# Optimization experiments

Measured on AMD Instinct MI355X. Metric: run time of the kernel, lower is better.

## Reference

```python
import jax, jax.numpy as jnp
import numpy as np

B, FEW, NN = 4096, 5, 64
D = 128            # embed_dim
NSYM = 100000
DM = 2 * D         # d_model = 256
DI = 2 * DM        # support-encoder inner = 512
H = 2 * DM         # LSTMCell hidden = 512
STEPS = 4          # process_steps


def setup_inputs() -> dict:
    key = jax.random.key(0)
    cnt = [0]
    def nk():
        cnt[0] += 1
        return jax.random.fold_in(key, cnt[0])
    def nrm(shape, scale=0.05):
        return jax.random.normal(nk(), shape, dtype=jnp.float32) * scale
    def ridx(shape):
        return jax.random.randint(nk(), shape, 0, NSYM, dtype=jnp.int32)
    inp = {}
    inp['q_l1'] = ridx((B, NN, 2)); inp['q_l2'] = ridx((B, NN, 2))
    inp['q_r1'] = ridx((B, NN, 2)); inp['q_r2'] = ridx((B, NN, 2))
    inp['s_l1'] = ridx((FEW, NN, 2)); inp['s_l2'] = ridx((FEW, NN, 2))
    inp['s_r1'] = ridx((FEW, NN, 2)); inp['s_r2'] = ridx((FEW, NN, 2))
    inp['q_deg_l'] = jax.random.randint(nk(), (B,), 1, NN, dtype=jnp.int32)
    inp['q_deg_r'] = jax.random.randint(nk(), (B,), 1, NN, dtype=jnp.int32)
    inp['s_deg_l'] = jax.random.randint(nk(), (FEW,), 1, NN, dtype=jnp.int32)
    inp['s_deg_r'] = jax.random.randint(nk(), (FEW,), 1, NN, dtype=jnp.int32)
    inp['emb'] = nrm((NSYM + 1, D)).at[NSYM].set(0.0)  # padding_idx row = 0
    inp['gcn_w'] = nrm((D, 2 * D))
    inp['gcn_wb'] = nrm((D,))
    inp['gcn_b'] = jnp.zeros((D,), jnp.float32)
    inp['hop_gate'] = jnp.ones((2,), jnp.float32)
    inp['attn_w'] = nrm((1, D))
    inp['attn_b'] = jnp.zeros((1,), jnp.float32)
    inp['p1_w'] = nrm((DI, DM)); inp['p1_b'] = jnp.zeros((DI,), jnp.float32)
    inp['p2_w'] = nrm((DM, DI)); inp['p2_b'] = jnp.zeros((DM,), jnp.float32)
    inp['ln_g'] = jnp.ones((DM,), jnp.float32); inp['ln_b'] = jnp.zeros((DM,), jnp.float32)
    inp['w_ih'] = nrm((4 * H, DM)); inp['w_hh'] = nrm((4 * H, H))
    inp['b_ih'] = jnp.zeros((4 * H,), jnp.float32); inp['b_hh'] = jnp.zeros((4 * H,), jnp.float32)
    return inp


def _neighbor_encoder(conn, emb, gcn_w, gcn_wb, gcn_b, attn_w, attn_b):
    # conn: [N, NN, 2] (relation id, entity id)
    e = emb[conn]                                     # [N, NN, 2, D]
    concat = e.reshape(conn.shape[0], conn.shape[1], 2 * D)  # cat(rel, ent)
    proj = concat @ gcn_w.T + gcn_wb + gcn_b          # [N, NN, D]
    scores = (proj @ attn_w.T + attn_b)[..., 0]       # [N, NN]
    w = jax.nn.softmax(scores, axis=1)[..., None]
    return jnp.tanh(jnp.sum(proj * w, axis=1))        # [N, D]


def _support_encoder(x, p1_w, p1_b, p2_w, p2_b, ln_g, ln_b):
    out = jax.nn.relu(x @ p1_w.T + p1_b) @ p2_w.T + p2_b
    z = out + x
    mu = jnp.mean(z, axis=-1, keepdims=True)
    var = jnp.var(z, axis=-1, keepdims=True)
    return (z - mu) / jnp.sqrt(var + 1e-6) * ln_g + ln_b


def _query_encoder(support_g, q, w_ih, w_hh, b_ih, b_hh):
    # matching-networks 'process' LSTM attention, STEPS fixed iterations
    h_r = jnp.zeros((q.shape[0], H), q.dtype)
    c = jnp.zeros_like(h_r)
    h = q
    for _ in range(STEPS):
        gates = q @ w_ih.T + b_ih + h_r @ w_hh.T + b_hh
        i, f, g, o = jnp.split(gates, 4, axis=-1)
        c = jax.nn.sigmoid(f) * c + jax.nn.sigmoid(i) * jnp.tanh(g)
        h_cell = jax.nn.sigmoid(o) * jnp.tanh(c)
        h = q + h_cell[:, :DM]
        attn = jax.nn.softmax(h @ support_g.T, axis=1)
        r = attn @ support_g
        h_r = jnp.concatenate([h, r], axis=1)
    return h


def reference(q_l1, q_l2, q_r1, q_r2, s_l1, s_l2, s_r1, s_r2,
              q_deg_l, q_deg_r, s_deg_l, s_deg_r,
              emb, gcn_w, gcn_wb, gcn_b, hop_gate, attn_w, attn_b,
              p1_w, p1_b, p2_w, p2_b, ln_g, ln_b, w_ih, w_hh, b_ih, b_hh):
    ne = lambda conn: _neighbor_encoder(conn, emb, gcn_w, gcn_wb, gcn_b, attn_w, attn_b)
    gw = jax.nn.softmax(hop_gate)
    q_left = gw[0] * ne(q_l1) + gw[1] * ne(q_l2)
    q_right = gw[0] * ne(q_r1) + gw[1] * ne(q_r2)
    s_left = gw[0] * ne(s_l1) + gw[1] * ne(s_l2)
    s_right = gw[0] * ne(s_r1) + gw[1] * ne(s_r2)
    query_neighbor = jnp.concatenate([q_left, q_right], axis=-1)    # [B, DM]
    support_neighbor = jnp.concatenate([s_left, s_right], axis=-1)  # [FEW, DM]
    support_g = _support_encoder(support_neighbor, p1_w, p1_b, p2_w, p2_b, ln_g, ln_b)
    query_g = _query_encoder(support_g, query_neighbor, w_ih, w_hh, b_ih, b_hh)
    support_m = jnp.mean(support_g, axis=0, keepdims=True)          # [1, DM]
    return (query_g @ support_m.T)[:, 0]                            # [B]
```

## Files before the change

### kernel.cpp

```cpp
#include <hip/hip_runtime.h>

typedef unsigned short bf16u;
typedef unsigned char u8;
typedef unsigned int u32;
typedef float f32x4 __attribute__((ext_vector_type(4)));
typedef short bf16x8 __attribute__((ext_vector_type(8)));

__device__ inline float sigmoidf_(float x) { return 1.f / (1.f + __expf(-x)); }
__device__ inline float tanhf_(float x) {
  float e = __expf(2.f * x);
  return 1.f - 2.f / (e + 1.f);
}
__device__ inline float b2f(bf16u u) { return __uint_as_float(((u32)u) << 16); }
__device__ inline bf16u f2b(float f) {
  u32 i = __float_as_uint(f);
  u32 r = (i + 0x7fffu + ((i >> 16) & 1u)) >> 16;
  return (bf16u)r;
}
__device__ inline u8 enc8(float v) {
  float q = fmaf(v, 512.f, 128.5f);
  q = fminf(fmaxf(q, 0.f), 255.f);
  return (u8)(int)q;
}
__device__ inline float ub0(u32 u) { return (float)(u & 0xffu); }
__device__ inline float ub1(u32 u) { return (float)((u >> 8) & 0xffu); }
__device__ inline float ub2(u32 u) { return (float)((u >> 16) & 0xffu); }
__device__ inline float ub3(u32 u) { return (float)(u >> 24); }

#define GLOAD16(gsrc, ldst)                                                   \
  __builtin_amdgcn_global_load_lds(                                           \
      (const __attribute__((address_space(1))) void*)(gsrc),                  \
      (__attribute__((address_space(3))) void*)(ldst), 16, 0, 0)

__global__ __launch_bounds__(256) void k_front(
    const float* __restrict__ emb, const float* __restrict__ gcn_w,
    const float* __restrict__ attn_w,
    const float* __restrict__ w_ih, const float* __restrict__ w_hh,
    const float* __restrict__ b_ih, const float* __restrict__ b_hh,
    u8* __restrict__ pr, u8* __restrict__ pe,
    float* __restrict__ srel, float* __restrict__ sent,
    bf16u* __restrict__ WWa, bf16u* __restrict__ WWb, float* __restrict__ bsum,
    bf16u* __restrict__ XX)
{
  const int blk = blockIdx.x, t = threadIdx.x;
  if (blk >= 1563) {
    const int b = blk - 1563;
    if (t < 59) {
      XX[(size_t)b * 576 + 517 + t] = 0;
      XX[(size_t)(b + 2048) * 576 + 517 + t] = 0;
    }
    float wi = w_ih[b * 256 + t];
    float wh = w_hh[b * 512 + t];
    WWa[(size_t)b * 576 + t] = f2b(wi);
    WWb[(size_t)b * 576 + t] = f2b(wi + wh);
    WWb[(size_t)b * 576 + 256 + t] = f2b(wh);
    if (t < 59) WWb[(size_t)b * 576 + 517 + t] = 0;
    if (t == 0) bsum[b] = b_ih[b] + b_hh[b];
    return;
  }
  const int row0 = blk << 6;
  __shared__ short As[64][136];
  __shared__ union PB {
    short B[128][136];
    u8 ob[64][272];
  } pb;
  __shared__ float us[256];
  {
    float acc = 0.f;
    #pragma unroll 8
    for (int d = 0; d < 128; ++d) acc = fmaf(gcn_w[d * 256 + t], attn_w[d], acc);
    us[t] = acc;
  }
  {
    #pragma unroll
    for (int s = 0; s < 8; ++s) {
      int f = s * 256 + t;
      int row = f >> 4, e0 = (f & 15) * 8;
      float4 v0 = *(const float4*)&gcn_w[row * 256 + e0];
      float4 v1 = *(const float4*)&gcn_w[row * 256 + e0 + 4];
      ushort4 p0, p1;
      p0.x = f2b(v0.x); p0.y = f2b(v0.y); p0.z = f2b(v0.z); p0.w = f2b(v0.w);
      p1.x = f2b(v1.x); p1.y = f2b(v1.y); p1.z = f2b(v1.z); p1.w = f2b(v1.w);
      *(ushort4*)&pb.B[row][e0] = p0;
      *(ushort4*)&pb.B[row][e0 + 4] = p1;
    }
  }
  #pragma unroll
  for (int s = 0; s < 8; ++s) {
    int f = s * 256 + t;
    int row = f >> 5, q = f & 31;
    int gr = row0 + row; if (gr > 100000) gr = 100000;
    float4 v = *(const float4*)&emb[(size_t)gr * 128 + (q << 2)];
    ushort4 pk;
    pk.x = f2b(v.x); pk.y = f2b(v.y); pk.z = f2b(v.z); pk.w = f2b(v.w);
    *(ushort4*)&As[row][q << 2] = pk;
  }
  __syncthreads();
  {
    const int row = t >> 2, l = t & 3;
    int gr = row0 + row; if (gr > 100000) gr = 100000;
    const short* ar = &As[row][l * 32];
    const float* u0 = &us[l * 32];
    const float* u1 = &us[128 + l * 32];
    float p0 = 0.f, p1 = 0.f;
    #pragma unroll
    for (int i = 0; i < 32; ++i) {
      float e = __uint_as_float(((u32)(unsigned short)ar[i]) << 16);
      p0 += e * u0[i];
      p1 += e * u1[i];
    }
    p0 += __shfl_xor(p0, 1, 64); p0 += __shfl_xor(p0, 2, 64);
    p1 += __shfl_xor(p1, 1, 64); p1 += __shfl_xor(p1, 2, 64);
    if (l == 0) { srel[gr] = p0; sent[gr] = p1; }
  }
  const int wave = t >> 6, lane = t & 63;
  const int quad = lane >> 4, l16 = lane & 15;
  const int wm = (wave >> 1) << 5, wn = (wave & 1) << 6;
  f32x4 acc0[2][4], acc1[2][4];
  #pragma unroll
  for (int i = 0; i < 2; ++i)
    #pragma unroll
    for (int j = 0; j < 4; ++j) {
      acc0[i][j] = (f32x4){0.f, 0.f, 0.f, 0.f};
      acc1[i][j] = (f32x4){0.f, 0.f, 0.f, 0.f};
    }
  #pragma unroll
  for (int kc = 0; kc < 4; ++kc) {
    bf16x8 af[2], bfr[4];
    #pragma unroll
    for (int i = 0; i < 2; ++i)
      af[i] = *(const bf16x8*)&As[wm + i * 16 + l16][kc * 32 + quad * 8];
    #pragma unroll
    for (int j = 0; j < 4; ++j)
      bfr[j] = *(const bf16x8*)&pb.B[wn + j * 16 + l16][kc * 32 + quad * 8];
    #pragma unroll
    for (int i = 0; i < 2; ++i)
      #pragma unroll
      for (int j = 0; j < 4; ++j)
        acc0[i][j] = __builtin_amdgcn_mfma_f32_16x16x32_bf16(af[i], bfr[j], acc0[i][j], 0, 0, 0);
  }
  __syncthreads();
  {
    #pragma unroll
    for (int s = 0; s < 8; ++s) {
      int f = s * 256 + t;
      int row = f >> 4, e0 = (f & 15) * 8;
      float4 v0 = *(const float4*)&gcn_w[row * 256 + 128 + e0];
      float4 v1 = *(const float4*)&gcn_w[row * 256 + 128 + e0 + 4];
      ushort4 p0, p1;
      p0.x = f2b(v0.x); p0.y = f2b(v0.y); p0.z = f2b(v0.z); p0.w = f2b(v0.w);
      p1.x = f2b(v1.x); p1.y = f2b(v1.y); p1.z = f2b(v1.z); p1.w = f2b(v1.w);
      *(ushort4*)&pb.B[row][e0] = p0;
      *(ushort4*)&pb.B[row][e0 + 4] = p1;
    }
  }
  __syncthreads();
  #pragma unroll
  for (int kc = 0; kc < 4; ++kc) {
    bf16x8 af[2], bfr[4];
    #pragma unroll
    for (int i = 0; i < 2; ++i)
      af[i] = *(const bf16x8*)&As[wm + i * 16 + l16][kc * 32 + quad * 8];
    #pragma unroll
    for (int j = 0; j < 4; ++j)
      bfr[j] = *(const bf16x8*)&pb.B[wn + j * 16 + l16][kc * 32 + quad * 8];
    #pragma unroll
    for (int i = 0; i < 2; ++i)
      #pragma unroll
      for (int j = 0; j < 4; ++j)
        acc1[i][j] = __builtin_amdgcn_mfma_f32_16x16x32_bf16(af[i], bfr[j], acc1[i][j], 0, 0, 0);
  }
  __syncthreads();
  #pragma unroll
  for (int j = 0; j < 4; ++j) {
    const int col = wn + j * 16 + l16;
    #pragma unroll
    for (int i = 0; i < 2; ++i) {
      #pragma unroll
      for (int r = 0; r < 4; ++r) {
        int row = wm + i * 16 + quad * 4 + r;
        pb.ob[row][col] = enc8(acc0[i][j][r]);
        pb.ob[row][128 + col] = enc8(acc1[i][j][r]);
      }
    }
  }
  __syncthreads();
  #pragma unroll
  for (int s = 0; s < 4; ++s) {
    int c = s * 256 + t;
    int row = c >> 4, part = c & 15;
    int gr = row0 + row;
    if (gr <= 100000) {
      uint4 v = *(const uint4*)&pb.ob[row][part * 16];
      if (part < 8) *(uint4*)&pr[(size_t)gr * 128 + part * 16] = v;
      else          *(uint4*)&pe[(size_t)gr * 128 + (part - 8) * 16] = v;
    }
  }
}

__global__ __launch_bounds__(256) void k_neighbor(
    const int* __restrict__ q_l1, const int* __restrict__ q_l2,
    const int* __restrict__ q_r1, const int* __restrict__ q_r2,
    const int* __restrict__ s_l1, const int* __restrict__ s_l2,
    const int* __restrict__ s_r1, const int* __restrict__ s_r2,
    const u8* __restrict__ pr, const u8* __restrict__ pe,
    const float* __restrict__ srel, const float* __restrict__ sent,
    const float* __restrict__ gcn_wb, const float* __restrict__ gcn_b,
    const float* __restrict__ hop_gate,
    float* __restrict__ qn, float* __restrict__ sn, bf16u* __restrict__ XX)
{
  const int b = blockIdx.x, t = threadIdx.x;
  const int *cA, *cB; float* outp; bf16u* xxp; int n, coloff;
  if (b < 4096)      { cA = q_l1; cB = q_l2; n = b;        outp = qn; xxp = XX; coloff = 0; }
  else if (b < 8192) { cA = q_r1; cB = q_r2; n = b - 4096; outp = qn; xxp = XX; coloff = 128; }
  else if (b < 8197) { cA = s_l1; cB = s_l2; n = b - 8192; outp = sn; xxp = 0;  coloff = 0; }
  else               { cA = s_r1; cB = s_r2; n = b - 8197; outp = sn; xxp = 0;  coloff = 128; }

  __shared__ float wS[2][64];
  __shared__ float red[256][17];

  const int hop = t >> 7, g = (t >> 3) & 15, p = t & 7;
  const int* connG = hop ? cB : cA;

  int2 pairs[4];
  #pragma unroll
  for (int kk = 0; kk < 4; ++kk)
    pairs[kk] = *(const int2*)&connG[(n * 64 + g + (kk << 4)) * 2];

  float vR = 0.f, vE = 0.f;
  if (t < 128) {
    const int sh = t >> 6, nn = t & 63;
    const int* connS = sh ? cB : cA;
    int2 sp = *(const int2*)&connS[(n * 64 + nn) * 2];
    vR = srel[sp.x];
    vE = sent[sp.y];
  }

  uint4 ra[4], rb[4];
  #pragma unroll
  for (int kk = 0; kk < 4; ++kk) {
    ra[kk] = *(const uint4*)&pr[(size_t)pairs[kk].x * 128 + p * 16];
    rb[kk] = *(const uint4*)&pe[(size_t)pairs[kk].y * 128 + p * 16];
  }

  if (t < 128) {
    const int sh = t >> 6, nn = t & 63;
    float sc = vR + vE;
    float m = sc;
    #pragma unroll
    for (int off = 32; off; off >>= 1) m = fmaxf(m, __shfl_xor(m, off, 64));
    float e = __expf(sc - m);
    float s = e;
    #pragma unroll
    for (int off = 32; off; off >>= 1) s += __shfl_xor(s, off, 64);
    wS[sh][nn] = e / s;
  }
  __syncthreads();

  float a[16];
  #pragma unroll
  for (int c = 0; c < 16; ++c) a[c] = 0.f;
  #pragma unroll
  for (int kk = 0; kk < 4; ++kk) {
    const float wk = wS[hop][g + (kk << 4)];
    const uint4 A = ra[kk], Bv = rb[kk];
    a[0]  += wk * (ub0(A.x) + ub0(Bv.x));
    a[1]  += wk * (ub1(A.x) + ub1(Bv.x));
    a[2]  += wk * (ub2(A.x) + ub2(Bv.x));
    a[3]  += wk * (ub3(A.x) + ub3(Bv.x));
    a[4]  += wk * (ub0(A.y) + ub0(Bv.y));
    a[5]  += wk * (ub1(A.y) + ub1(Bv.y));
    a[6]  += wk * (ub2(A.y) + ub2(Bv.y));
    a[7]  += wk * (ub3(A.y) + ub3(Bv.y));
    a[8]  += wk * (ub0(A.z) + ub0(Bv.z));
    a[9]  += wk * (ub1(A.z) + ub1(Bv.z));
    a[10] += wk * (ub2(A.z) + ub2(Bv.z));
    a[11] += wk * (ub3(A.z) + ub3(Bv.z));
    a[12] += wk * (ub0(A.w) + ub0(Bv.w));
    a[13] += wk * (ub1(A.w) + ub1(Bv.w));
    a[14] += wk * (ub2(A.w) + ub2(Bv.w));
    a[15] += wk * (ub3(A.w) + ub3(Bv.w));
  }
  #pragma unroll
  for (int c = 0; c < 16; ++c) red[t][c] = a[c];
  __syncthreads();

  if (t < 128) {
    const int d = t, pp = d >> 4, cc = d & 15;
    float sA = 0.f, sB = 0.f;
    #pragma unroll
    for (int gg = 0; gg < 16; ++gg) {
      sA += red[gg * 8 + pp][cc];
      sB += red[128 + gg * 8 + pp][cc];
    }
    float accA = sA * (1.f / 512.f) - 0.5f;
    float accB = sB * (1.f / 512.f) - 0.5f;
    float bias = gcn_wb[d] + gcn_b[d];
    float g0 = hop_gate[0], g1 = hop_gate[1];
    float mx = fmaxf(g0, g1);
    float e0 = __expf(g0 - mx), e1 = __expf(g1 - mx);
    float inv = 1.f / (e0 + e1);
    float v = e0 * inv * tanhf_(bias + accA) + e1 * inv * tanhf_(bias + accB);
    outp[n * 256 + coloff + d] = v;
    if (xxp) xxp[(size_t)n * 576 + coloff + d] = f2b(v);
  }
}

__global__ __launch_bounds__(256) void k_sup1(
    const float* __restrict__ sn, const float* __restrict__ p1_w,
    const float* __restrict__ p1_b, float* __restrict__ h1)
{
  const int r = blockIdx.x >> 3, j0 = (blockIdx.x & 7) << 6;
  const int t = threadIdx.x;
  __shared__ float xs[256];
  xs[t] = sn[r * 256 + t];
  __syncthreads();
  const int j = j0 + (t >> 2), q = t & 3;
  const float* wr = p1_w + (size_t)j * 256 + q * 64;
  float acc = 0.f;
  #pragma unroll
  for (int k = 0; k < 64; ++k) acc += xs[q * 64 + k] * wr[k];
  acc += __shfl_xor(acc, 1, 64);
  acc += __shfl_xor(acc, 2, 64);
  if (q == 0) h1[r * 512 + j] = fmaxf(acc + p1_b[j], 0.f);
}

__global__ __launch_bounds__(256) void k_sup2(
    const float* __restrict__ sn, const float* __restrict__ h1,
    const float* __restrict__ p2_w, const float* __restrict__ p2_b,
    const float* __restrict__ ln_g, const float* __restrict__ ln_b,
    float* __restrict__ sg)
{
  const int r = blockIdx.x, t = threadIdx.x;
  const int lane = t & 63, wave = t >> 6;
  __shared__ float hs[512];
  __shared__ float zs[256];
  __shared__ float r1[4], r2[4];
  hs[t] = h1[r * 512 + t];
  hs[t + 256] = h1[r * 512 + 256 + t];
  __syncthreads();
  const int q = t & 3;
  #pragma unroll
  for (int jc = 0; jc < 4; ++jc) {
    int j = jc * 64 + (t >> 2);
    const float* wr = p2_w + (size_t)j * 512 + q * 128;
    float acc = 0.f;
    #pragma unroll
    for (int k = 0; k < 128; ++k) acc += hs[q * 128 + k] * wr[k];
    acc += __shfl_xor(acc, 1, 64);
    acc += __shfl_xor(acc, 2, 64);
    if (q == 0) zs[j] = acc + p2_b[j] + sn[r * 256 + j];
  }
  __syncthreads();
  float v = zs[t];
  float s1 = v, s2 = v * v;
  #pragma unroll
  for (int off = 32; off; off >>= 1) { s1 += __shfl_xor(s1, off, 64); s2 += __shfl_xor(s2, off, 64); }
  if (lane == 0) { r1[wave] = s1; r2[wave] = s2; }
  __syncthreads();
  float S1 = r1[0] + r1[1] + r1[2] + r1[3];
  float S2 = r2[0] + r2[1] + r2[2] + r2[3];
  float mu = S1 * (1.f / 256.f);
  float var = S2 * (1.f / 256.f) - mu * mu;
  sg[r * 256 + t] = (v - mu) * rsqrtf(var + 1e-6f) * ln_g[t] + ln_b[t];
}

__global__ __launch_bounds__(256) void k_sg2(
    const float* __restrict__ sg, const float* __restrict__ w_hh,
    bf16u* __restrict__ WWb, float* __restrict__ sm)
{
  __shared__ float s[5][256];
  const int t = threadIdx.x;
  for (int i = t; i < 1280; i += 256) s[i >> 8][i & 255] = sg[i];
  __syncthreads();
  if (blockIdx.x == 0)
    sm[t] = (s[0][t] + s[1][t] + s[2][t] + s[3][t] + s[4][t]) * 0.2f;
  const int j = (blockIdx.x << 6) + (t >> 2), q = t & 3;
  const float4* wr = (const float4*)(w_hh + (size_t)j * 512 + 256 + q * 64);
  float a[5] = {0.f, 0.f, 0.f, 0.f, 0.f};
  #pragma unroll
  for (int kk = 0; kk < 16; ++kk) {
    float4 w = wr[kk];
    int k = q * 64 + kk * 4;
    #pragma unroll
    for (int r = 0; r < 5; ++r)
      a[r] += s[r][k] * w.x + s[r][k+1] * w.y + s[r][k+2] * w.z + s[r][k+3] * w.w;
  }
  #pragma unroll
  for (int r = 0; r < 5; ++r) {
    a[r] += __shfl_xor(a[r], 1, 64);
    a[r] += __shfl_xor(a[r], 2, 64);
  }
  if (q == 0) {
    #pragma unroll
    for (int r = 0; r < 5; ++r)
      WWb[(size_t)j * 576 + 512 + r] = f2b(a[r]);
  }
}

__global__ __launch_bounds__(256) void k_gates_mfma(
    const bf16u* __restrict__ XX, const bf16u* __restrict__ WW,
    const float* __restrict__ bsum, bf16u* __restrict__ gates, int kchunks)
{
  const int t = threadIdx.x;
  const int wave = t >> 6, lane = t & 63;
  const int quad = lane >> 4, l16 = lane & 15;
  const int wm = (wave >> 1) << 6, wn = (wave & 1) << 6;
  const int lin = (blockIdx.x & 7) * 56 + (blockIdx.x >> 3);
  const int row0 = (lin / 14) << 7;
  const int col0 = (lin % 14) << 7;
  __shared__ short As[2][128][64];
  __shared__ short Bs[2][128][64];
  f32x4 acc[4][4];
  #pragma unroll
  for (int i = 0; i < 4; ++i)
    #pragma unroll
    for (int j = 0; j < 4; ++j) acc[i][j] = (f32x4){0.f, 0.f, 0.f, 0.f};

  int offX[4], offW[4];
  #pragma unroll
  for (int e = 0; e < 4; ++e) {
    int row = wave * 32 + e * 8 + (lane >> 3);
    int sw = (lane & 7) ^ (lane >> 3);
    offX[e] = (row0 + row) * 576 + sw * 8;
    offW[e] = (col0 + row) * 576 + sw * 8;
  }
  char* aBase = (char*)&As[0][0][0] + wave * 4096;
  char* bBase = (char*)&Bs[0][0][0] + wave * 4096;

  #define STAGE(buf, kc)                                                      \
    {                                                                         \
      const int kof_ = (kc) * 64;                                             \
      _Pragma("unroll")                                                       \
      for (int e = 0; e < 4; ++e) {                                           \
        GLOAD16(XX + offX[e] + kof_, aBase + (buf) * 16384 + e * 1024);       \
        GLOAD16(WW + offW[e] + kof_, bBase + (buf) * 16384 + e * 1024);       \
      }                                                                       \
    }

  STAGE(0, 0);
  __syncthreads();

  for (int kc = 0; kc < kchunks; ++kc) {
    const int cur = kc & 1;
    if (kc + 1 < kchunks) STAGE(cur ^ 1, kc + 1);
    #pragma unroll
    for (int kc2 = 0; kc2 < 2; ++kc2) {
      bf16x8 af[4], bfr[4];
      #pragma unroll
      for (int i = 0; i < 4; ++i)
        af[i] = *(const bf16x8*)&As[cur][wm + i * 16 + l16]
                                       [(((kc2 << 2) + quad) ^ (l16 & 7)) << 3];
      #pragma unroll
      for (int j = 0; j < 4; ++j)
        bfr[j] = *(const bf16x8*)&Bs[cur][wn + j * 16 + l16]
                                        [(((kc2 << 2) + quad) ^ (l16 & 7)) << 3];
      #pragma unroll
      for (int i = 0; i < 4; ++i)
        #pragma unroll
        for (int j = 0; j < 4; ++j)
          acc[i][j] = __builtin_amdgcn_mfma_f32_16x16x32_bf16(af[i], bfr[j], acc[i][j], 0, 0, 0);
    }
    __syncthreads();
  }
  #undef STAGE

  #pragma unroll
  for (int j = 0; j < 4; ++j) {
    const int col = col0 + wn + j * 16 + l16;
    const float bs = bsum[col];
    #pragma unroll
    for (int i = 0; i < 4; ++i) {
      #pragma unroll
      for (int r = 0; r < 4; ++r) {
        int row = row0 + wm + i * 16 + quad * 4 + r;
        gates[(size_t)row * 2048 + col] = f2b(acc[i][j][r] + bs);
      }
    }
  }
}

__global__ __launch_bounds__(256) void k_cell(
    const bf16u* __restrict__ gates, const float* __restrict__ qn,
    float* __restrict__ c, bf16u* __restrict__ XX,
    const float* __restrict__ sg, const float* __restrict__ sm,
    float* __restrict__ out, int step)
{
  __shared__ float red[4][6];
  const int b = blockIdx.x, t = threadIdx.x;
  const int lane = t & 63, wave = t >> 6;
  const bf16u* g = gates + (size_t)b * 2048;
  float i0 = b2f(g[t]),       f0 = b2f(g[512 + t]), gg0 = b2f(g[1024 + t]), o0 = b2f(g[1536 + t]);
  float i1 = b2f(g[256 + t]), f1 = b2f(g[768 + t]), gg1 = b2f(g[1280 + t]);
  float co0 = step ? c[b * 512 + t] : 0.f;
  float co1 = step ? c[b * 512 + 256 + t] : 0.f;
  float c0 = sigmoidf_(f0) * co0 + sigmoidf_(i0) * tanhf_(gg0);
  float c1 = sigmoidf_(f1) * co1 + sigmoidf_(i1) * tanhf_(gg1);
  if (step < 3) {
    c[b * 512 + t] = c0;
    c[b * 512 + 256 + t] = c1;
  }
  float hcv = sigmoidf_(o0) * tanhf_(c0);
  float h = qn[b * 256 + t] + hcv;
  if (step < 3) {
    XX[(size_t)b * 576 + 256 + t] = f2b(hcv);
    float dots[5];
    #pragma unroll
    for (int s = 0; s < 5; ++s) dots[s] = h * sg[s * 256 + t];
    #pragma unroll
    for (int off = 32; off; off >>= 1) {
      #pragma unroll
      for (int s = 0; s < 5; ++s) dots[s] += __shfl_xor(dots[s], off, 64);
    }
    if (lane == 0) {
      #pragma unroll
      for (int s = 0; s < 5; ++s) red[wave][s] = dots[s];
    }
    __syncthreads();
    #pragma unroll
    for (int s = 0; s < 5; ++s)
      dots[s] = red[0][s] + red[1][s] + red[2][s] + red[3][s];
    float m = dots[0];
    #pragma unroll
    for (int s = 1; s < 5; ++s) m = fmaxf(m, dots[s]);
    float sum = 0.f;
    #pragma unroll
    for (int s = 0; s < 5; ++s) sum += __expf(dots[s] - m);
    if (t < 5) {
      float dv = (t == 1) ? dots[1] : (t == 2) ? dots[2] : (t == 3) ? dots[3]
               : (t == 4) ? dots[4] : dots[0];
      XX[(size_t)b * 576 + 512 + t] = f2b(__expf(dv - m) / sum);
    }
  } else {
    float v = h * sm[t];
    #pragma unroll
    for (int off = 32; off; off >>= 1) v += __shfl_xor(v, off, 64);
    if (lane == 0) red[wave][0] = v;
    __syncthreads();
    if (t == 0) out[b] = red[0][0] + red[1][0] + red[2][0] + red[3][0];
  }
}

extern "C" void kernel_launch(void* const* d_in, const int* in_sizes, int n_in,
                              void* d_out, int out_size, void* d_ws, size_t ws_size,
                              hipStream_t stream)
{
  (void)in_sizes; (void)n_in; (void)out_size; (void)ws_size;
  const int *q_l1 = (const int*)d_in[0], *q_l2 = (const int*)d_in[1];
  const int *q_r1 = (const int*)d_in[2], *q_r2 = (const int*)d_in[3];
  const int *s_l1 = (const int*)d_in[4], *s_l2 = (const int*)d_in[5];
  const int *s_r1 = (const int*)d_in[6], *s_r2 = (const int*)d_in[7];
  const float* emb      = (const float*)d_in[12];
  const float* gcn_w    = (const float*)d_in[13];
  const float* gcn_wb   = (const float*)d_in[14];
  const float* gcn_b    = (const float*)d_in[15];
  const float* hop_gate = (const float*)d_in[16];
  const float* attn_w   = (const float*)d_in[17];
  const float* p1_w = (const float*)d_in[19];
  const float* p1_b = (const float*)d_in[20];
  const float* p2_w = (const float*)d_in[21];
  const float* p2_b = (const float*)d_in[22];
  const float* ln_g = (const float*)d_in[23];
  const float* ln_b = (const float*)d_in[24];
  const float* w_ih = (const float*)d_in[25];
  const float* w_hh = (const float*)d_in[26];
  const float* b_ih = (const float*)d_in[27];
  const float* b_hh = (const float*)d_in[28];

  char* base = (char*)d_ws;
  size_t off = 0;
  auto alloc = [&](size_t bytes) -> char* {
    char* r = base + off;
    off = (off + bytes + 255) & ~(size_t)255;
    return r;
  };
  u8* pr       = (u8*)alloc(100001ull * 128);
  u8* pe       = (u8*)alloc(100001ull * 128);
  float* srel  = (float*)alloc(100001ull * 4);
  float* sent  = (float*)alloc(100001ull * 4);
  float* qn    = (float*)alloc(4096ull * 256 * 4);
  float* sn    = (float*)alloc(5 * 256 * 4);
  float* sg    = (float*)alloc(5 * 256 * 4);
  float* sm    = (float*)alloc(256 * 4);
  float* h1b   = (float*)alloc(5 * 512 * 4);
  bf16u* XX    = (bf16u*)alloc(4096ull * 576 * 2);
  bf16u* WWa   = (bf16u*)alloc(2048ull * 576 * 2);
  bf16u* WWb   = (bf16u*)alloc(2048ull * 576 * 2);
  float* bsum  = (float*)alloc(2048 * 4);
  bf16u* gates = (bf16u*)alloc(4096ull * 2048 * 2);
  float* cbuf  = (float*)alloc(4096ull * 512 * 4);

  k_front<<<3611, 256, 0, stream>>>(emb, gcn_w, attn_w, w_ih, w_hh, b_ih, b_hh,
                                    pr, pe, srel, sent, WWa, WWb, bsum, XX);
  k_neighbor<<<8202, 256, 0, stream>>>(q_l1, q_l2, q_r1, q_r2, s_l1, s_l2, s_r1, s_r2,
                                       pr, pe, srel, sent, gcn_wb, gcn_b, hop_gate,
                                       qn, sn, XX);
  k_sup1<<<40, 256, 0, stream>>>(sn, p1_w, p1_b, h1b);
  k_sup2<<<5, 256, 0, stream>>>(sn, h1b, p2_w, p2_b, ln_g, ln_b, sg);
  k_sg2<<<32, 256, 0, stream>>>(sg, w_hh, WWb, sm);

  for (int step = 0; step < 4; ++step) {
    if (step == 0)
      k_gates_mfma<<<448, 256, 0, stream>>>(XX, WWa, bsum, gates, 4);
    else
      k_gates_mfma<<<448, 256, 0, stream>>>(XX, WWb, bsum, gates, 9);
    k_cell<<<4096, 256, 0, stream>>>(gates, qn, cbuf, XX, sg, sm, (float*)d_out, step);
  }
}
```

Before: 335.7 us.

## Fuse support-encoder kernels and fold sg2 into first gates launch; reuse bf16 gcn_w

Merges k_sup1 and k_sup2 into a single 5-block kernel, and moves the k_sg2 work (support mean and the w_hh·sg columns) into the first 32 blocks of the step-0 gates GEMM. That removes three small serial launches and their launch gaps. In k_front, the attention projection vector is now computed from the bf16 gcn_w tile already in shared memory instead of strided global reads, and that work is interleaved with the MFMA phases. The trade-offs are that us is now built from bf16-rounded weights (slight precision change) and that the 32 fused blocks in the gates kernel carry extra serial work.

New measurement: 345.3 us. 1.03x slower.

```diff
diff --git a/kernel.cpp b/kernel.cpp
--- a/kernel.cpp
+++ b/kernel.cpp
@@ -65,25 +65,17 @@
     u8 ob[64][272];
   } pb;
   __shared__ float us[256];
-  {
-    float acc = 0.f;
-    #pragma unroll 8
-    for (int d = 0; d < 128; ++d) acc = fmaf(gcn_w[d * 256 + t], attn_w[d], acc);
-    us[t] = acc;
-  }
-  {
-    #pragma unroll
-    for (int s = 0; s < 8; ++s) {
-      int f = s * 256 + t;
-      int row = f >> 4, e0 = (f & 15) * 8;
-      float4 v0 = *(const float4*)&gcn_w[row * 256 + e0];
-      float4 v1 = *(const float4*)&gcn_w[row * 256 + e0 + 4];
-      ushort4 p0, p1;
-      p0.x = f2b(v0.x); p0.y = f2b(v0.y); p0.z = f2b(v0.z); p0.w = f2b(v0.w);
-      p1.x = f2b(v1.x); p1.y = f2b(v1.y); p1.z = f2b(v1.z); p1.w = f2b(v1.w);
-      *(ushort4*)&pb.B[row][e0] = p0;
-      *(ushort4*)&pb.B[row][e0 + 4] = p1;
-    }
+  #pragma unroll
+  for (int s = 0; s < 8; ++s) {
+    int f = s * 256 + t;
+    int row = f >> 4, e0 = (f & 15) * 8;
+    float4 v0 = *(const float4*)&gcn_w[row * 256 + e0];
+    float4 v1 = *(const float4*)&gcn_w[row * 256 + e0 + 4];
+    ushort4 p0, p1;
+    p0.x = f2b(v0.x); p0.y = f2b(v0.y); p0.z = f2b(v0.z); p0.w = f2b(v0.w);
+    p1.x = f2b(v1.x); p1.y = f2b(v1.y); p1.z = f2b(v1.z); p1.w = f2b(v1.w);
+    *(ushort4*)&pb.B[row][e0] = p0;
+    *(ushort4*)&pb.B[row][e0 + 4] = p1;
   }
   #pragma unroll
   for (int s = 0; s < 8; ++s) {
@@ -96,6 +88,78 @@
     *(ushort4*)&As[row][q << 2] = pk;
   }
   __syncthreads();
+  if (t < 128) {
+    float a = 0.f;
+    #pragma unroll 8
+    for (int d = 0; d < 128; ++d)
+      a = fmaf(__uint_as_float(((u32)(unsigned short)pb.B[d][t]) << 16),
+               attn_w[d], a);
+    us[t] = a;
+  }
+  const int wave = t >> 6, lane = t & 63;
+  const int quad = lane >> 4, l16 = lane & 15;
+  const int wm = (wave >> 1) << 5, wn = (wave & 1) << 6;
+  f32x4 acc0[2][4], acc1[2][4];
+  #pragma unroll
+  for (int i = 0; i < 2; ++i)
+    #pragma unroll
+    for (int j = 0; j < 4; ++j) {
+      acc0[i][j] = (f32x4){0.f, 0.f, 0.f, 0.f};
+      acc1[i][j] = (f32x4){0.f, 0.f, 0.f, 0.f};
+    }
+  #pragma unroll
+  for (int kc = 0; kc < 4; ++kc) {
+    bf16x8 af[2], bfr[4];
+    #pragma unroll
+    for (int i = 0; i < 2; ++i)
+      af[i] = *(const bf16x8*)&As[wm + i * 16 + l16][kc * 32 + quad * 8];
+    #pragma unroll
+    for (int j = 0; j < 4; ++j)
+      bfr[j] = *(const bf16x8*)&pb.B[wn + j * 16 + l16][kc * 32 + quad * 8];
+    #pragma unroll
+    for (int i = 0; i < 2; ++i)
+      #pragma unroll
+      for (int j = 0; j < 4; ++j)
+        acc0[i][j] = __builtin_amdgcn_mfma_f32_16x16x32_bf16(af[i], bfr[j], acc0[i][j], 0, 0, 0);
+  }
+  __syncthreads();
+  #pragma unroll
+  for (int s = 0; s < 8; ++s) {
+    int f = s * 256 + t;
+    int row = f >> 4, e0 = (f & 15) * 8;
+    float4 v0 = *(const float4*)&gcn_w[row * 256 + 128 + e0];
+    float4 v1 = *(const float4*)&gcn_w[row * 256 + 128 + e0 + 4];
+    ushort4 p0, p1;
+    p0.x = f2b(v0.x); p0.y = f2b(v0.y); p0.z = f2b(v0.z); p0.w = f2b(v0.w);
+    p1.x = f2b(v1.x); p1.y = f2b(v1.y); p1.z = f2b(v1.z); p1.w = f2b(v1.w);
+    *(ushort4*)&pb.B[row][e0] = p0;
+    *(ushort4*)&pb.B[row][e0 + 4] = p1;
+  }
+  __syncthreads();
+  if (t < 128) {
+    float a = 0.f;
+    #pragma unroll 8
+    for (int d = 0; d < 128; ++d)
+      a = fmaf(__uint_as_float(((u32)(unsigned short)pb.B[d][t]) << 16),
+               attn_w[d], a);
+    us[128 + t] = a;
+  }
+  #pragma unroll
+  for (int kc = 0; kc < 4; ++kc) {
+    bf16x8 af[2], bfr[4];
+    #pragma unroll
+    for (int i = 0; i < 2; ++i)
+      af[i] = *(const bf16x8*)&As[wm + i * 16 + l16][kc * 32 + quad * 8];
+    #pragma unroll
+    for (int j = 0; j < 4; ++j)
+      bfr[j] = *(const bf16x8*)&pb.B[wn + j * 16 + l16][kc * 32 + quad * 8];
+    #pragma unroll
+    for (int i = 0; i < 2; ++i)
+      #pragma unroll
+      for (int j = 0; j < 4; ++j)
+        acc1[i][j] = __builtin_amdgcn_mfma_f32_16x16x32_bf16(af[i], bfr[j], acc1[i][j], 0, 0, 0);
+  }
+  __syncthreads();
   {
     const int row = t >> 2, l = t & 3;
     int gr = row0 + row; if (gr > 100000) gr = 100000;
@@ -113,64 +177,6 @@
     p1 += __shfl_xor(p1, 1, 64); p1 += __shfl_xor(p1, 2, 64);
     if (l == 0) { srel[gr] = p0; sent[gr] = p1; }
   }
-  const int wave = t >> 6, lane = t & 63;
-  const int quad = lane >> 4, l16 = lane & 15;
-  const int wm = (wave >> 1) << 5, wn = (wave & 1) << 6;
-  f32x4 acc0[2][4], acc1[2][4];
-  #pragma unroll
-  for (int i = 0; i < 2; ++i)
-    #pragma unroll
-    for (int j = 0; j < 4; ++j) {
-      acc0[i][j] = (f32x4){0.f, 0.f, 0.f, 0.f};
-      acc1[i][j] = (f32x4){0.f, 0.f, 0.f, 0.f};
-    }
-  #pragma unroll
-  for (int kc = 0; kc < 4; ++kc) {
-    bf16x8 af[2], bfr[4];
-    #pragma unroll
-    for (int i = 0; i < 2; ++i)
-      af[i] = *(const bf16x8*)&As[wm + i * 16 + l16][kc * 32 + quad * 8];
-    #pragma unroll
-    for (int j = 0; j < 4; ++j)
-      bfr[j] = *(const bf16x8*)&pb.B[wn + j * 16 + l16][kc * 32 + quad * 8];
-    #pragma unroll
-    for (int i = 0; i < 2; ++i)
-      #pragma unroll
-      for (int j = 0; j < 4; ++j)
-        acc0[i][j] = __builtin_amdgcn_mfma_f32_16x16x32_bf16(af[i], bfr[j], acc0[i][j], 0, 0, 0);
-  }
-  __syncthreads();
-  {
-    #pragma unroll
-    for (int s = 0; s < 8; ++s) {
-      int f = s * 256 + t;
-      int row = f >> 4, e0 = (f & 15) * 8;
-      float4 v0 = *(const float4*)&gcn_w[row * 256 + 128 + e0];
-      float4 v1 = *(const float4*)&gcn_w[row * 256 + 128 + e0 + 4];
-      ushort4 p0, p1;
-      p0.x = f2b(v0.x); p0.y = f2b(v0.y); p0.z = f2b(v0.z); p0.w = f2b(v0.w);
-      p1.x = f2b(v1.x); p1.y = f2b(v1.y); p1.z = f2b(v1.z); p1.w = f2b(v1.w);
-      *(ushort4*)&pb.B[row][e0] = p0;
-      *(ushort4*)&pb.B[row][e0 + 4] = p1;
-    }
-  }
-  __syncthreads();
-  #pragma unroll
-  for (int kc = 0; kc < 4; ++kc) {
-    bf16x8 af[2], bfr[4];
-    #pragma unroll
-    for (int i = 0; i < 2; ++i)
-      af[i] = *(const bf16x8*)&As[wm + i * 16 + l16][kc * 32 + quad * 8];
-    #pragma unroll
-    for (int j = 0; j < 4; ++j)
-      bfr[j] = *(const bf16x8*)&pb.B[wn + j * 16 + l16][kc * 32 + quad * 8];
-    #pragma unroll
-    for (int i = 0; i < 2; ++i)
-      #pragma unroll
-      for (int j = 0; j < 4; ++j)
-        acc1[i][j] = __builtin_amdgcn_mfma_f32_16x16x32_bf16(af[i], bfr[j], acc1[i][j], 0, 0, 0);
-  }
-  __syncthreads();
   #pragma unroll
   for (int j = 0; j < 4; ++j) {
     const int col = wn + j * 16 + l16;
@@ -306,38 +312,33 @@
   }
 }
 
-__global__ __launch_bounds__(256) void k_sup1(
+__global__ __launch_bounds__(256) void k_sup(
     const float* __restrict__ sn, const float* __restrict__ p1_w,
-    const float* __restrict__ p1_b, float* __restrict__ h1)
-{
-  const int r = blockIdx.x >> 3, j0 = (blockIdx.x & 7) << 6;
-  const int t = threadIdx.x;
-  __shared__ float xs[256];
-  xs[t] = sn[r * 256 + t];
-  __syncthreads();
-  const int j = j0 + (t >> 2), q = t & 3;
-  const float* wr = p1_w + (size_t)j * 256 + q * 64;
-  float acc = 0.f;
-  #pragma unroll
-  for (int k = 0; k < 64; ++k) acc += xs[q * 64 + k] * wr[k];
-  acc += __shfl_xor(acc, 1, 64);
-  acc += __shfl_xor(acc, 2, 64);
-  if (q == 0) h1[r * 512 + j] = fmaxf(acc + p1_b[j], 0.f);
-}
-
-__global__ __launch_bounds__(256) void k_sup2(
-    const float* __restrict__ sn, const float* __restrict__ h1,
-    const float* __restrict__ p2_w, const float* __restrict__ p2_b,
-    const float* __restrict__ ln_g, const float* __restrict__ ln_b,
-    float* __restrict__ sg)
+    const float* __restrict__ p1_b, const float* __restrict__ p2_w,
+    const float* __restrict__ p2_b, const float* __restrict__ ln_g,
+    const float* __restrict__ ln_b, float* __restrict__ sg)
 {
   const int r = blockIdx.x, t = threadIdx.x;
   const int lane = t & 63, wave = t >> 6;
+  __shared__ float xs[256];
   __shared__ float hs[512];
   __shared__ float zs[256];
   __shared__ float r1[4], r2[4];
-  hs[t] = h1[r * 512 + t];
-  hs[t + 256] = h1[r * 512 + 256 + t];
+  xs[t] = sn[r * 256 + t];
+  __syncthreads();
+  #pragma unroll
+  for (int jj = 0; jj < 2; ++jj) {
+    const int j = t + jj * 256;
+    const float4* wr = (const float4*)(p1_w + (size_t)j * 256);
+    float acc = 0.f;
+    #pragma unroll
+    for (int k = 0; k < 64; ++k) {
+      float4 w = wr[k];
+      acc += xs[k * 4] * w.x + xs[k * 4 + 1] * w.y +
+             xs[k * 4 + 2] * w.z + xs[k * 4 + 3] * w.w;
+    }
+    hs[j] = fmaxf(acc + p1_b[j], 0.f);
+  }
   __syncthreads();
   const int q = t & 3;
   #pragma unroll
@@ -349,7 +350,7 @@
     for (int k = 0; k < 128; ++k) acc += hs[q * 128 + k] * wr[k];
     acc += __shfl_xor(acc, 1, 64);
     acc += __shfl_xor(acc, 2, 64);
-    if (q == 0) zs[j] = acc + p2_b[j] + sn[r * 256 + j];
+    if (q == 0) zs[j] = acc + p2_b[j] + xs[j];
   }
   __syncthreads();
   float v = zs[t];
@@ -365,42 +366,11 @@
   sg[r * 256 + t] = (v - mu) * rsqrtf(var + 1e-6f) * ln_g[t] + ln_b[t];
 }
 
-__global__ __launch_bounds__(256) void k_sg2(
-    const float* __restrict__ sg, const float* __restrict__ w_hh,
-    bf16u* __restrict__ WWb, float* __restrict__ sm)
-{
-  __shared__ float s[5][256];
-  const int t = threadIdx.x;
-  for (int i = t; i < 1280; i += 256) s[i >> 8][i & 255] = sg[i];
-  __syncthreads();
-  if (blockIdx.x == 0)
-    sm[t] = (s[0][t] + s[1][t] + s[2][t] + s[3][t] + s[4][t]) * 0.2f;
-  const int j = (blockIdx.x << 6) + (t >> 2), q = t & 3;
-  const float4* wr = (const float4*)(w_hh + (size_t)j * 512 + 256 + q * 64);
-  float a[5] = {0.f, 0.f, 0.f, 0.f, 0.f};
-  #pragma unroll
-  for (int kk = 0; kk < 16; ++kk) {
-    float4 w = wr[kk];
-    int k = q * 64 + kk * 4;
-    #pragma unroll
-    for (int r = 0; r < 5; ++r)
-      a[r] += s[r][k] * w.x + s[r][k+1] * w.y + s[r][k+2] * w.z + s[r][k+3] * w.w;
-  }
-  #pragma unroll
-  for (int r = 0; r < 5; ++r) {
-    a[r] += __shfl_xor(a[r], 1, 64);
-    a[r] += __shfl_xor(a[r], 2, 64);
-  }
-  if (q == 0) {
-    #pragma unroll
-    for (int r = 0; r < 5; ++r)
-      WWb[(size_t)j * 576 + 512 + r] = f2b(a[r]);
-  }
-}
-
 __global__ __launch_bounds__(256) void k_gates_mfma(
     const bf16u* __restrict__ XX, const bf16u* __restrict__ WW,
-    const float* __restrict__ bsum, bf16u* __restrict__ gates, int kchunks)
+    const float* __restrict__ bsum, bf16u* __restrict__ gates, int kchunks,
+    const float* __restrict__ sg, const float* __restrict__ w_hh,
+    bf16u* __restrict__ WWbo, float* __restrict__ sm, int dosg2)
 {
   const int t = threadIdx.x;
   const int wave = t >> 6, lane = t & 63;
@@ -411,6 +381,38 @@
   const int col0 = (lin % 14) << 7;
   __shared__ short As[2][128][64];
   __shared__ short Bs[2][128][64];
+
+  if (dosg2 && blockIdx.x < 32) {
+    float (*s5)[256] = (float(*)[256])&As[0][0][0];
+    const int blk = blockIdx.x;
+    for (int i = t; i < 1280; i += 256) s5[i >> 8][i & 255] = sg[i];
+    __syncthreads();
+    if (blk == 0)
+      sm[t] = (s5[0][t] + s5[1][t] + s5[2][t] + s5[3][t] + s5[4][t]) * 0.2f;
+    const int j = (blk << 6) + (t >> 2), q = t & 3;
+    const float4* wr = (const float4*)(w_hh + (size_t)j * 512 + 256 + q * 64);
+    float a[5] = {0.f, 0.f, 0.f, 0.f, 0.f};
+    #pragma unroll
+    for (int kk = 0; kk < 16; ++kk) {
+      float4 w = wr[kk];
+      int k = q * 64 + kk * 4;
+      #pragma unroll
+      for (int r = 0; r < 5; ++r)
+        a[r] += s5[r][k] * w.x + s5[r][k+1] * w.y + s5[r][k+2] * w.z + s5[r][k+3] * w.w;
+    }
+    #pragma unroll
+    for (int r = 0; r < 5; ++r) {
+      a[r] += __shfl_xor(a[r], 1, 64);
+      a[r] += __shfl_xor(a[r], 2, 64);
+    }
+    if (q == 0) {
+      #pragma unroll
+      for (int r = 0; r < 5; ++r)
+        WWbo[(size_t)j * 576 + 512 + r] = f2b(a[r]);
+    }
+    __syncthreads();
+  }
+
   f32x4 acc[4][4];
   #pragma unroll
   for (int i = 0; i < 4; ++i)
@@ -582,7 +584,6 @@
   float* sn    = (float*)alloc(5 * 256 * 4);
   float* sg    = (float*)alloc(5 * 256 * 4);
   float* sm    = (float*)alloc(256 * 4);
-  float* h1b   = (float*)alloc(5 * 512 * 4);
   bf16u* XX    = (bf16u*)alloc(4096ull * 576 * 2);
   bf16u* WWa   = (bf16u*)alloc(2048ull * 576 * 2);
   bf16u* WWb   = (bf16u*)alloc(2048ull * 576 * 2);
@@ -595,15 +596,15 @@
   k_neighbor<<<8202, 256, 0, stream>>>(q_l1, q_l2, q_r1, q_r2, s_l1, s_l2, s_r1, s_r2,
                                        pr, pe, srel, sent, gcn_wb, gcn_b, hop_gate,
                                        qn, sn, XX);
-  k_sup1<<<40, 256, 0, stream>>>(sn, p1_w, p1_b, h1b);
-  k_sup2<<<5, 256, 0, stream>>>(sn, h1b, p2_w, p2_b, ln_g, ln_b, sg);
-  k_sg2<<<32, 256, 0, stream>>>(sg, w_hh, WWb, sm);
+  k_sup<<<5, 256, 0, stream>>>(sn, p1_w, p1_b, p2_w, p2_b, ln_g, ln_b, sg);
 
   for (int step = 0; step < 4; ++step) {
     if (step == 0)
-      k_gates_mfma<<<448, 256, 0, stream>>>(XX, WWa, bsum, gates, 4);
+      k_gates_mfma<<<448, 256, 0, stream>>>(XX, WWa, bsum, gates, 4,
+                                            sg, w_hh, WWb, sm, 1);
     else
-      k_gates_mfma<<<448, 256, 0, stream>>>(XX, WWb, bsum, gates, 9);
+      k_gates_mfma<<<448, 256, 0, stream>>>(XX, WWb, bsum, gates, 9,
+                                            sg, w_hh, WWb, sm, 0);
     k_cell<<<4096, 256, 0, stream>>>(gates, qn, cbuf, XX, sg, sm, (float*)d_out, step);
   }
 }
```
